# Optimization experiments

Hardware: AMD Instinct MI355X
Metric: run time of the kernel (lower is better)

## Reference

```python
import jax, jax.numpy as jnp
import numpy as np

SCALES = (1, 2, 4)
KS = 5          # conv kernel size
POOL = 2        # maxpool kernel & stride


def coarse_grain(x, s):
    # non-overlapping mean pool along last axis
    B, C, L = x.shape
    Lc = L // s
    return x[:, :, : Lc * s].reshape(B, C, Lc, s).mean(axis=-1)


def conv1d(x, w, b):
    # x: [B, C_in, L], w: [C_out, C_in, K] (torch layout), VALID padding, stride 1
    y = jax.lax.conv_general_dilated(
        x, w, window_strides=(1,), padding='VALID',
        dimension_numbers=('NCH', 'OIH', 'NCH'))
    return y + b[None, :, None]


def maxpool1d(x, k):
    B, C, L = x.shape
    Lp = L // k
    return x[:, :, : Lp * k].reshape(B, C, Lp, k).max(axis=-1)


def conv_block(x, w1, b1, w2, b2):
    x = maxpool1d(jax.nn.relu(conv1d(x, w1, b1)), POOL)
    x = maxpool1d(jax.nn.relu(conv1d(x, w2, b2)), POOL)
    return x


def setup_inputs() -> dict:
    key = jax.random.key(0)
    ks = jax.random.split(key, 9)
    B, C, NWL = 2048, 4, 480
    C1, C2 = 16, 32
    # flatten size per model's own arithmetic: sum over scales of conv/pool output lens * C2
    F = (117 + 57 + 27) * C2  # 6432
    NOUT = 5
    sc = lambda fan_in: 1.0 / np.sqrt(fan_in)
    return {
        'x':  jax.random.normal(ks[0], (B, C, NWL), dtype=jnp.float32),
        'w1': jax.random.uniform(ks[1], (C1, C, KS), jnp.float32, -sc(C * KS), sc(C * KS)),
        'b1': jax.random.uniform(ks[2], (C1,), jnp.float32, -sc(C * KS), sc(C * KS)),
        'w2': jax.random.uniform(ks[3], (C2, C1, KS), jnp.float32, -sc(C1 * KS), sc(C1 * KS)),
        'b2': jax.random.uniform(ks[4], (C2,), jnp.float32, -sc(C1 * KS), sc(C1 * KS)),
        'wl': jax.random.uniform(ks[5], (F, F), jnp.float32, -sc(F), sc(F)),
        'bl': jax.random.uniform(ks[6], (F,), jnp.float32, -sc(F), sc(F)),
        'wo': jax.random.uniform(ks[7], (NOUT, F), jnp.float32, -sc(F), sc(F)),
        'bo': jax.random.uniform(ks[8], (NOUT,), jnp.float32, -sc(F), sc(F)),
    }


def reference(x, w1, b1, w2, b2, wl, bl, wo, bo):
    # multi-scale feature mapping: shared ConvBlock applied to each coarse-grained scale
    feats = [conv_block(coarse_grain(x, s), w1, b1, w2, b2) for s in SCALES]
    f = jnp.concatenate(feats, axis=-1)            # [B, 32, 201]
    f = f.reshape(f.shape[0], -1)                  # [B, 6432]
    # the SAME linear layer (shared weights) is applied 4 times in torch
    for _ in range(4):
        f = jax.nn.relu(f @ wl.T + bl)
    return f @ wo.T + bo                           # [B, 5]
```

## Files before the change

### kernel.cpp

```cpp
#include <hip/hip_runtime.h>

typedef _Float16 v8h __attribute__((ext_vector_type(8)));
typedef _Float16 v4h __attribute__((ext_vector_type(4)));
typedef float    v4f __attribute__((ext_vector_type(4)));

#define GK 6432
#define GN 6432
#define GM 2048
#define KP 6528

__global__ void convert_w(const float* __restrict__ wl, _Float16* __restrict__ Wh)
{
    const int row = blockIdx.y;
    const int col = (blockIdx.x * 256 + threadIdx.x) * 4;
    if (col >= KP) return;
    v4h h;
    if (col < GK) {
        const float4 f = *(const float4*)(wl + (long)row * GK + col);
        h[0] = (_Float16)f.x; h[1] = (_Float16)f.y;
        h[2] = (_Float16)f.z; h[3] = (_Float16)f.w;
    } else {
        h[0] = (_Float16)0.f; h[1] = (_Float16)0.f;
        h[2] = (_Float16)0.f; h[3] = (_Float16)0.f;
    }
    *(v4h*)(Wh + (long)row * KP + col) = h;
}

#define SX   0
#define SX2  2048
#define SX4  3136
#define SW1  3712
#define SB1  4032
#define SW2  4048
#define SB2  6608
#define SP1  6640
#define LDSZ 13808

__global__ __launch_bounds__(256) void conv_feat(
    const float* __restrict__ x,
    const float* __restrict__ w1, const float* __restrict__ b1,
    const float* __restrict__ w2, const float* __restrict__ b2,
    _Float16* __restrict__ F0)
{
    __shared__ float lds[LDSZ];
    const int tid = threadIdx.x;
    const long b  = blockIdx.x;

    for (int i = tid; i < 1920; i += 256) {
        int c = i / 480, t = i % 480;
        lds[SX + c * 512 + t] = x[(b * 4 + c) * 480 + t];
    }
    for (int i = tid; i < 320;  i += 256) lds[SW1 + i] = w1[i];
    for (int i = tid; i < 16;   i += 256) lds[SB1 + i] = b1[i];
    for (int i = tid; i < 2560; i += 256) lds[SW2 + i] = w2[i];
    for (int i = tid; i < 32;   i += 256) lds[SB2 + i] = b2[i];
    for (int i = tid; i < KP - GK; i += 256) F0[b * KP + GK + i] = (_Float16)0.f;
    __syncthreads();

    for (int i = tid; i < 960; i += 256) {
        int c = i / 240, t = i % 240;
        lds[SX2 + c * 272 + t] = 0.5f * (lds[SX + c * 512 + 2 * t] + lds[SX + c * 512 + 2 * t + 1]);
    }
    for (int i = tid; i < 480; i += 256) {
        int c = i / 120, t = i % 120;
        float s = lds[SX + c * 512 + 4 * t]     + lds[SX + c * 512 + 4 * t + 1]
                + lds[SX + c * 512 + 4 * t + 2] + lds[SX + c * 512 + 4 * t + 3];
        lds[SX4 + c * 144 + t] = 0.25f * s;
    }
    __syncthreads();

    for (int jid = tid; jid < 16 * 34; jid += 256) {
        const int c1 = jid / 34, rid = jid % 34;
        const int sidx = (rid < 19) ? 0 : (rid < 29 ? 1 : 2);
        const int r0   = (sidx == 0) ? rid : (sidx == 1 ? rid - 19 : rid - 29);
        const int u0   = r0 * 13;
        const int xbase  = (sidx == 0) ? SX  : (sidx == 1 ? SX2 : SX4);
        const int xpitch = (sidx == 0) ? 512 : (sidx == 1 ? 272 : 144);
        const int P      = (sidx == 0) ? 238 : (sidx == 1 ? 118 : 58);
        const int pofs   = (sidx == 0) ? 0   : (sidx == 1 ? 238 : 356);

        float acc[26];
        const float bias = lds[SB1 + c1];
        #pragma unroll
        for (int i = 0; i < 26; ++i) acc[i] = bias;

        #pragma unroll
        for (int ci = 0; ci < 4; ++ci) {
            float w[30];
            const float* xr = &lds[xbase + ci * xpitch + 2 * u0];
            #pragma unroll
            for (int q = 0; q < 15; ++q) {
                float2 t2 = *(const float2*)(xr + 2 * q);
                w[2 * q] = t2.x; w[2 * q + 1] = t2.y;
            }
            float wt[5];
            #pragma unroll
            for (int k = 0; k < 5; ++k) wt[k] = lds[SW1 + (c1 * 4 + ci) * 5 + k];
            #pragma unroll
            for (int i = 0; i < 26; ++i) {
                #pragma unroll
                for (int k = 0; k < 5; ++k) acc[i] += w[i + k] * wt[k];
            }
        }
        #pragma unroll
        for (int i = 0; i < 13; ++i) {
            int u = u0 + i;
            if (u < P)
                lds[SP1 + c1 * 448 + pofs + u] = fmaxf(fmaxf(acc[2 * i], acc[2 * i + 1]), 0.f);
        }
    }
    __syncthreads();

    for (int jid = tid; jid < 32 * 17; jid += 256) {
        const int c2 = jid / 17, rid = jid % 17;
        const int sidx = (rid < 9) ? 0 : (rid < 14 ? 1 : 2);
        const int r0   = (sidx == 0) ? rid : (sidx == 1 ? rid - 9 : rid - 14);
        const int v0   = r0 * 13;
        const int pbase = (sidx == 0) ? 0   : (sidx == 1 ? 238 : 356);
        const int Pv    = (sidx == 0) ? 117 : (sidx == 1 ? 57  : 27);
        const int vout  = (sidx == 0) ? 0   : (sidx == 1 ? 117 : 174);

        float acc[26];
        const float bias = lds[SB2 + c2];
        #pragma unroll
        for (int i = 0; i < 26; ++i) acc[i] = bias;

        for (int c1 = 0; c1 < 16; ++c1) {
            float w[30];
            const float* pr = &lds[SP1 + c1 * 448 + pbase + 2 * v0];
            #pragma unroll
            for (int q = 0; q < 15; ++q) {
                float2 t2 = *(const float2*)(pr + 2 * q);
                w[2 * q] = t2.x; w[2 * q + 1] = t2.y;
            }
            float wt[5];
            #pragma unroll
            for (int k = 0; k < 5; ++k) wt[k] = lds[SW2 + (c2 * 16 + c1) * 5 + k];
            #pragma unroll
            for (int i = 0; i < 26; ++i) {
                #pragma unroll
                for (int k = 0; k < 5; ++k) acc[i] += w[i + k] * wt[k];
            }
        }
        #pragma unroll
        for (int i = 0; i < 13; ++i) {
            int v = v0 + i;
            if (v < Pv) {
                float f = fmaxf(fmaxf(acc[2 * i], acc[2 * i + 1]), 0.f);
                F0[b * KP + c2 * 201 + vout + v] = (_Float16)f;
            }
        }
    }
}

__global__ __launch_bounds__(1024, 4) void gemm16(
    const _Float16* __restrict__ A, const _Float16* __restrict__ Bw,
    const float* __restrict__ bias, _Float16* __restrict__ C)
{
    __shared__ _Float16 sA[2][256 * 64];
    __shared__ _Float16 sB[2][256 * 64];

    const int tid  = threadIdx.x;
    const int lane = tid & 63;
    const int wave = tid >> 6;
    const int wm   = wave >> 2;
    const int wn   = wave & 3;

    const int id = blockIdx.x;
    const long tile_m = (long)(id & 7) << 8;
    const long tile_n = (long)(id >> 3) << 8;

    const int lrow = lane >> 3;
    const int lcol = ((lane & 7) ^ lrow) << 3;

    const _Float16* pAst = A + (tile_m + wave * 16 + lrow) * (long)KP + lcol;
    const int dA0 = wave * 16 * 64, dA1 = dA0 + 512;

    const int bRow01 = (wave >> 2) * 64 + (wave & 3) * 8;
    long rb01 = tile_n + bRow01;
    long rb23 = rb01 + 32;
    long r01l = rb01 + lrow; if (r01l > 6431) r01l = 6431;
    long r23l = rb23 + lrow; if (r23l > 6431) r23l = 6431;
    const _Float16* pB01 = Bw + r01l * (long)KP + lcol;
    const _Float16* pB23 = Bw + r23l * (long)KP + lcol;
    const int dB01 = bRow01 * 64;
    const int dB23 = dB01 + 32 * 64;

#define GLD(p, d) __builtin_amdgcn_global_load_lds(                          \
        (const __attribute__((address_space(1))) void*)(p),                  \
        (__attribute__((address_space(3))) void*)(d), 16, 0, 0)

#define STAGE_A(CUR, q)   { GLD(q, &sA[CUR][dA0]); GLD((q) + 8L * KP, &sA[CUR][dA1]); }
#define STAGE_B01(CUR, q) { GLD(q, &sB[CUR][dB01]); }
#define STAGE_B23(CUR, q) { GLD(q, &sB[CUR][dB23]); }

    const int fr = lane & 15;
    const int fp = lane >> 4;
    const int sw = fr & 7;
    const int slot0 = ((fp)     ^ sw) << 3;
    const int slot1 = ((fp + 4) ^ sw) << 3;
    const int arow0 = wm * 64 + fr;
    const int brow0 = wn * 64 + fr;

    v8h af[4][2], bf0, bf1;
    v4f acc[4][4];
    #pragma unroll
    for (int mi = 0; mi < 4; ++mi) {
        #pragma unroll
        for (int nf = 0; nf < 4; ++nf) { v4f z = {0.f, 0.f, 0.f, 0.f}; acc[mi][nf] = z; }
    }

#define LDAALL(CUR) { _Pragma("unroll")                                      \
    for (int mi = 0; mi < 4; ++mi) {                                         \
        af[mi][0] = *(const v8h*)&sA[CUR][(arow0 + mi * 16) * 64 + slot0];   \
        af[mi][1] = *(const v8h*)&sA[CUR][(arow0 + mi * 16) * 64 + slot1];   \
    } }

#define LDB(CUR, P) {                                                        \
    bf0 = *(const v8h*)&sB[CUR][(brow0 + (P) * 16) * 64 + slot0];            \
    bf1 = *(const v8h*)&sB[CUR][(brow0 + (P) * 16) * 64 + slot1]; }

#define MMAP(P) { _Pragma("unroll")                                          \
    for (int mi = 0; mi < 4; ++mi) {                                         \
        acc[mi][P] = __builtin_amdgcn_mfma_f32_16x16x32_f16(af[mi][0], bf0,  \
                                                            acc[mi][P], 0, 0, 0); \
        acc[mi][P] = __builtin_amdgcn_mfma_f32_16x16x32_f16(af[mi][1], bf1,  \
                                                            acc[mi][P], 0, 0, 0); \
    } }

#define ROUND(CUR, S1, S2, VN) {                                             \
              \
    LDAALL(CUR); LDB(CUR, 0);                                                \
    if (S1) STAGE_B23((CUR) ^ 1, qB23);                                      \
    __builtin_amdgcn_s_barrier();                                            \
    asm volatile("s_waitcnt lgkmcnt(0)" ::: "memory");                       \
    __builtin_amdgcn_s_setprio(1);                                           \
    MMAP(0);                                                                 \
    __builtin_amdgcn_s_setprio(0);                                           \
    __builtin_amdgcn_s_barrier();                                            \
                             \
    LDB(CUR, 1);                                                             \
    if (S2) STAGE_A(CUR, qA);                                                \
    __builtin_amdgcn_s_barrier();                                            \
    asm volatile("s_waitcnt lgkmcnt(0)" ::: "memory");                       \
    __builtin_amdgcn_s_setprio(1);                                           \
    MMAP(1);                                                                 \
    __builtin_amdgcn_s_setprio(0);                                           \
    __builtin_amdgcn_s_barrier();                                            \
                          \
    LDB(CUR, 2);                                                             \
    if (S2) STAGE_B01(CUR, qB01);                                            \
    __builtin_amdgcn_s_barrier();                                            \
    asm volatile("s_waitcnt lgkmcnt(0)" ::: "memory");                       \
    __builtin_amdgcn_s_setprio(1);                                           \
    MMAP(2);                                                                 \
    __builtin_amdgcn_s_setprio(0);                                           \
    __builtin_amdgcn_s_barrier();                                            \
                                    \
    LDB(CUR, 3);                                                             \
    __builtin_amdgcn_s_barrier();                                            \
    asm volatile("s_waitcnt lgkmcnt(0)" ::: "memory");                       \
    __builtin_amdgcn_s_setprio(1);                                           \
    MMAP(3);                                                                 \
    __builtin_amdgcn_s_setprio(0);                                           \
    asm volatile("s_waitcnt vmcnt(" #VN ")" ::: "memory");                   \
    __builtin_amdgcn_s_barrier();                                            \
    qA += 64; qB01 += 64; qB23 += 64; }

    STAGE_A(0, pAst); STAGE_B01(0, pB01); STAGE_B23(0, pB23);
    STAGE_A(1, pAst + 64); STAGE_B01(1, pB01 + 64);
    asm volatile("s_waitcnt vmcnt(3)" ::: "memory");
    __builtin_amdgcn_s_barrier();

    const _Float16* qA   = pAst + 128;
    const _Float16* qB01 = pB01 + 128;
    const _Float16* qB23 = pB23 + 64;

    for (int kt = 0; kt < 100; kt += 2) {
        ROUND(0, 1, 1, 3);
        ROUND(1, 1, 1, 3);
    }
    ROUND(0, 1, 0, 0);
    ROUND(1, 0, 0, 0);

    #pragma unroll
    for (int nf = 0; nf < 4; ++nf) {
        const long col = tile_n + wn * 64 + nf * 16 + fr;
        if (col < KP) {
            const bool val = col < GN;
            const float bv = val ? bias[col] : 0.f;
            #pragma unroll
            for (int mi = 0; mi < 4; ++mi) {
                const long row = tile_m + wm * 64 + mi * 16 + fp * 4;
                #pragma unroll
                for (int r = 0; r < 4; ++r) {
                    float v = acc[mi][nf][r] + bv;
                    v = v > 0.f ? v : 0.f;
                    C[(row + r) * (long)KP + col] = val ? (_Float16)v : (_Float16)0.f;
                }
            }
        }
    }

#undef GLD
#undef STAGE_A
#undef STAGE_B01
#undef STAGE_B23
#undef LDAALL
#undef LDB
#undef MMAP
#undef ROUND
}

__global__ __launch_bounds__(256) void final_out(
    const _Float16* __restrict__ F, const float* __restrict__ wo,
    const float* __restrict__ bo, float* __restrict__ out)
{
    __shared__ float red[4][8];
    const long b   = blockIdx.x;
    const int tid  = threadIdx.x;
    const int lane = tid & 63;
    const int wave = tid >> 6;
    float acc[5] = {0.f, 0.f, 0.f, 0.f, 0.f};
    const _Float16* f = F + b * KP;

    const int c1 = (wave + 1) * 402;
    for (int c = wave * 402 + lane; c < c1; c += 64) {
        const int k = c << 2;
        v4h f4 = *(const v4h*)(f + k);
        const float f0 = (float)f4[0], f1 = (float)f4[1];
        const float f2 = (float)f4[2], f3 = (float)f4[3];
        #pragma unroll
        for (int o = 0; o < 5; ++o) {
            const float4 w4 = *(const float4*)(wo + o * GK + k);
            acc[o] += f0 * w4.x + f1 * w4.y + f2 * w4.z + f3 * w4.w;
        }
    }
    #pragma unroll
    for (int o = 0; o < 5; ++o) {
        #pragma unroll
        for (int off = 32; off > 0; off >>= 1) acc[o] += __shfl_down(acc[o], off, 64);
    }
    if (lane == 0) {
        #pragma unroll
        for (int o = 0; o < 5; ++o) red[wave][o] = acc[o];
    }
    __syncthreads();
    if (tid < 5)
        out[b * 5 + tid] = red[0][tid] + red[1][tid] + red[2][tid] + red[3][tid] + bo[tid];
}

extern "C" void kernel_launch(void* const* d_in, const int* in_sizes, int n_in,
                              void* d_out, int out_size, void* d_ws, size_t ws_size,
                              hipStream_t stream)
{
    const float* x  = (const float*)d_in[0];
    const float* w1 = (const float*)d_in[1];
    const float* b1 = (const float*)d_in[2];
    const float* w2 = (const float*)d_in[3];
    const float* b2 = (const float*)d_in[4];
    const float* wl = (const float*)d_in[5];
    const float* bl = (const float*)d_in[6];
    const float* wo = (const float*)d_in[7];
    const float* bo = (const float*)d_in[8];
    float* out = (float*)d_out;

    char* ws = (char*)d_ws;
    _Float16* Wh = (_Float16*)ws;
    _Float16* F0 = (_Float16*)(ws + 83976192);
    _Float16* F1 = (_Float16*)(ws + 83976192 + 26738688);

    convert_w<<<dim3(7, GN), 256, 0, stream>>>(wl, Wh);
    conv_feat<<<GM, 256, 0, stream>>>(x, w1, b1, w2, b2, F0);
    gemm16<<<208, 1024, 0, stream>>>(F0, Wh, bl, F1);
    gemm16<<<208, 1024, 0, stream>>>(F1, Wh, bl, F0);
    gemm16<<<208, 1024, 0, stream>>>(F0, Wh, bl, F1);
    gemm16<<<208, 1024, 0, stream>>>(F1, Wh, bl, F0);
    final_out<<<GM, 256, 0, stream>>>(F0, wo, bo, out);
}
```

Before: 1.179 ms.

## Fuse output projection into last GEMM epilogue and double-buffer B fragments

The final linear layer (5 outputs) moves into the epilogue of the fourth GEMM. Each tile applies bias and ReLU, dots the result with the wo slice staged in LDS, reduces across lanes, and atomically adds into an output that a small init kernel first fills with the bias. This removes the last activation write and the separate final_out kernel. The GEMM main loop also now loads the next B fragment into a second register pair before the current MFMAs and waits with lgkmcnt(2) instead of 0, overlapping LDS reads with matrix math. The cost is extra registers, nondeterministic float atomic summation order, and an added launch.

Measured after the change: 1.950 ms. +65.4%, slower.

```diff
diff --git a/kernel.cpp b/kernel.cpp
--- a/kernel.cpp
+++ b/kernel.cpp
@@ -153,9 +153,18 @@
     }
 }
 
+__global__ __launch_bounds__(512) void out_init(const float* __restrict__ bo,
+                                                float* __restrict__ out)
+{
+    const int i = blockIdx.x * 512 + threadIdx.x;
+    if (i < GM * 5) out[i] = bo[i % 5];
+}
+
+template<int FUSED>
 __global__ __launch_bounds__(1024, 4) void gemm16(
     const _Float16* __restrict__ A, const _Float16* __restrict__ Bw,
-    const float* __restrict__ bias, _Float16* __restrict__ C)
+    const float* __restrict__ bias, _Float16* __restrict__ C,
+    const float* __restrict__ wo, float* __restrict__ outp)
 {
     __shared__ _Float16 sA[2][256 * 64];
     __shared__ _Float16 sB[2][256 * 64];
@@ -202,7 +211,7 @@
     const int arow0 = wm * 64 + fr;
     const int brow0 = wn * 64 + fr;
 
-    v8h af[4][2], bf0, bf1;
+    v8h af[4][2], bA0, bA1, bB0, bB1;
     v4f acc[4][4];
     #pragma unroll
     for (int mi = 0; mi < 4; ++mi) {
@@ -216,52 +225,50 @@
         af[mi][1] = *(const v8h*)&sA[CUR][(arow0 + mi * 16) * 64 + slot1];   \
     } }
 
-#define LDB(CUR, P) {                                                        \
-    bf0 = *(const v8h*)&sB[CUR][(brow0 + (P) * 16) * 64 + slot0];            \
-    bf1 = *(const v8h*)&sB[CUR][(brow0 + (P) * 16) * 64 + slot1]; }
-
-#define MMAP(P) { _Pragma("unroll")                                          \
+#define LDB(CUR, P, D0, D1) {                                                \
+    D0 = *(const v8h*)&sB[CUR][(brow0 + (P) * 16) * 64 + slot0];             \
+    D1 = *(const v8h*)&sB[CUR][(brow0 + (P) * 16) * 64 + slot1]; }
+
+#define MMAP(P, B0, B1) { _Pragma("unroll")                                  \
     for (int mi = 0; mi < 4; ++mi) {                                         \
-        acc[mi][P] = __builtin_amdgcn_mfma_f32_16x16x32_f16(af[mi][0], bf0,  \
+        acc[mi][P] = __builtin_amdgcn_mfma_f32_16x16x32_f16(af[mi][0], B0,   \
                                                             acc[mi][P], 0, 0, 0); \
-        acc[mi][P] = __builtin_amdgcn_mfma_f32_16x16x32_f16(af[mi][1], bf1,  \
+        acc[mi][P] = __builtin_amdgcn_mfma_f32_16x16x32_f16(af[mi][1], B1,   \
                                                             acc[mi][P], 0, 0, 0); \
     } }
 
 #define ROUND(CUR, S1, S2, VN) {                                             \
-              \
-    LDAALL(CUR); LDB(CUR, 0);                                                \
+            \
+    LDAALL(CUR); LDB(CUR, 0, bA0, bA1); LDB(CUR, 1, bB0, bB1);               \
     if (S1) STAGE_B23((CUR) ^ 1, qB23);                                      \
     __builtin_amdgcn_s_barrier();                                            \
+    asm volatile("s_waitcnt lgkmcnt(2)" ::: "memory");                       \
+    __builtin_amdgcn_s_setprio(1);                                           \
+    MMAP(0, bA0, bA1);                                                       \
+    __builtin_amdgcn_s_setprio(0);                                           \
+    __builtin_amdgcn_s_barrier();                                            \
+                   \
+    LDB(CUR, 2, bA0, bA1);                                                   \
+    if (S2) STAGE_A(CUR, qA);                                                \
+    __builtin_amdgcn_s_barrier();                                            \
+    asm volatile("s_waitcnt lgkmcnt(2)" ::: "memory");                       \
+    __builtin_amdgcn_s_setprio(1);                                           \
+    MMAP(1, bB0, bB1);                                                       \
+    __builtin_amdgcn_s_setprio(0);                                           \
+    __builtin_amdgcn_s_barrier();                                            \
+                 \
+    LDB(CUR, 3, bB0, bB1);                                                   \
+    if (S2) STAGE_B01(CUR, qB01);                                            \
+    __builtin_amdgcn_s_barrier();                                            \
+    asm volatile("s_waitcnt lgkmcnt(2)" ::: "memory");                       \
+    __builtin_amdgcn_s_setprio(1);                                           \
+    MMAP(2, bA0, bA1);                                                       \
+    __builtin_amdgcn_s_setprio(0);                                           \
+    __builtin_amdgcn_s_barrier();                                            \
+               \
     asm volatile("s_waitcnt lgkmcnt(0)" ::: "memory");                       \
     __builtin_amdgcn_s_setprio(1);                                           \
-    MMAP(0);                                                                 \
-    __builtin_amdgcn_s_setprio(0);                                           \
-    __builtin_amdgcn_s_barrier();                                            \
-                             \
-    LDB(CUR, 1);                                                             \
-    if (S2) STAGE_A(CUR, qA);                                                \
-    __builtin_amdgcn_s_barrier();                                            \
-    asm volatile("s_waitcnt lgkmcnt(0)" ::: "memory");                       \
-    __builtin_amdgcn_s_setprio(1);                                           \
-    MMAP(1);                                                                 \
-    __builtin_amdgcn_s_setprio(0);                                           \
-    __builtin_amdgcn_s_barrier();                                            \
-                          \
-    LDB(CUR, 2);                                                             \
-    if (S2) STAGE_B01(CUR, qB01);                                            \
-    __builtin_amdgcn_s_barrier();                                            \
-    asm volatile("s_waitcnt lgkmcnt(0)" ::: "memory");                       \
-    __builtin_amdgcn_s_setprio(1);                                           \
-    MMAP(2);                                                                 \
-    __builtin_amdgcn_s_setprio(0);                                           \
-    __builtin_amdgcn_s_barrier();                                            \
-                                    \
-    LDB(CUR, 3);                                                             \
-    __builtin_amdgcn_s_barrier();                                            \
-    asm volatile("s_waitcnt lgkmcnt(0)" ::: "memory");                       \
-    __builtin_amdgcn_s_setprio(1);                                           \
-    MMAP(3);                                                                 \
+    MMAP(3, bB0, bB1);                                                       \
     __builtin_amdgcn_s_setprio(0);                                           \
     asm volatile("s_waitcnt vmcnt(" #VN ")" ::: "memory");                   \
     __builtin_amdgcn_s_barrier();                                            \
@@ -283,20 +290,69 @@
     ROUND(0, 1, 0, 0);
     ROUND(1, 0, 0, 0);
 
-    #pragma unroll
-    for (int nf = 0; nf < 4; ++nf) {
-        const long col = tile_n + wn * 64 + nf * 16 + fr;
-        if (col < KP) {
-            const bool val = col < GN;
-            const float bv = val ? bias[col] : 0.f;
-            #pragma unroll
-            for (int mi = 0; mi < 4; ++mi) {
-                const long row = tile_m + wm * 64 + mi * 16 + fp * 4;
-                #pragma unroll
-                for (int r = 0; r < 4; ++r) {
-                    float v = acc[mi][nf][r] + bv;
+    if constexpr (FUSED == 0) {
+        #pragma unroll
+        for (int nf = 0; nf < 4; ++nf) {
+            const long col = tile_n + wn * 64 + nf * 16 + fr;
+            if (col < KP) {
+                const bool val = col < GN;
+                const float bv = val ? bias[col] : 0.f;
+                #pragma unroll
+                for (int mi = 0; mi < 4; ++mi) {
+                    const long row = tile_m + wm * 64 + mi * 16 + fp * 4;
+                    #pragma unroll
+                    for (int r = 0; r < 4; ++r) {
+                        float v = acc[mi][nf][r] + bv;
+                        v = v > 0.f ? v : 0.f;
+                        C[(row + r) * (long)KP + col] = val ? (_Float16)v : (_Float16)0.f;
+                    }
+                }
+            }
+        }
+    } else {
+        float* fl = (float*)&sA[0][0];
+        __syncthreads();
+        for (int i = tid; i < 256 * 6; i += 1024) {
+            const int c = i & 255, j = i >> 8;
+            const long gcol = tile_n + c;
+            float v = 0.f;
+            if (gcol < GN) v = (j == 0) ? bias[gcol] : wo[(long)(j - 1) * GK + gcol];
+            fl[j * 256 + c] = v;
+        }
+        __syncthreads();
+        const float* biasL = fl;
+        const float* woL   = fl + 256;
+        #pragma unroll
+        for (int mi = 0; mi < 4; ++mi) {
+            #pragma unroll
+            for (int r = 0; r < 4; ++r) {
+                float s0 = 0.f, s1 = 0.f, s2 = 0.f, s3 = 0.f, s4 = 0.f;
+                #pragma unroll
+                for (int nf = 0; nf < 4; ++nf) {
+                    const int cl = wn * 64 + nf * 16 + fr;
+                    float v = acc[mi][nf][r] + biasL[cl];
                     v = v > 0.f ? v : 0.f;
-                    C[(row + r) * (long)KP + col] = val ? (_Float16)v : (_Float16)0.f;
+                    s0 += v * woL[cl];
+                    s1 += v * woL[256 + cl];
+                    s2 += v * woL[512 + cl];
+                    s3 += v * woL[768 + cl];
+                    s4 += v * woL[1024 + cl];
+                }
+                #pragma unroll
+                for (int m = 1; m < 16; m <<= 1) {
+                    s0 += __shfl_xor(s0, m, 64);
+                    s1 += __shfl_xor(s1, m, 64);
+                    s2 += __shfl_xor(s2, m, 64);
+                    s3 += __shfl_xor(s3, m, 64);
+                    s4 += __shfl_xor(s4, m, 64);
+                }
+                if (fr == 0) {
+                    const long row = tile_m + wm * 64 + mi * 16 + fp * 4 + r;
+                    atomicAdd(&outp[row * 5 + 0], s0);
+                    atomicAdd(&outp[row * 5 + 1], s1);
+                    atomicAdd(&outp[row * 5 + 2], s2);
+                    atomicAdd(&outp[row * 5 + 3], s3);
+                    atomicAdd(&outp[row * 5 + 4], s4);
                 }
             }
         }
@@ -310,44 +366,6 @@
 #undef LDB
 #undef MMAP
 #undef ROUND
-}
-
-__global__ __launch_bounds__(256) void final_out(
-    const _Float16* __restrict__ F, const float* __restrict__ wo,
-    const float* __restrict__ bo, float* __restrict__ out)
-{
-    __shared__ float red[4][8];
-    const long b   = blockIdx.x;
-    const int tid  = threadIdx.x;
-    const int lane = tid & 63;
-    const int wave = tid >> 6;
-    float acc[5] = {0.f, 0.f, 0.f, 0.f, 0.f};
-    const _Float16* f = F + b * KP;
-
-    const int c1 = (wave + 1) * 402;
-    for (int c = wave * 402 + lane; c < c1; c += 64) {
-        const int k = c << 2;
-        v4h f4 = *(const v4h*)(f + k);
-        const float f0 = (float)f4[0], f1 = (float)f4[1];
-        const float f2 = (float)f4[2], f3 = (float)f4[3];
-        #pragma unroll
-        for (int o = 0; o < 5; ++o) {
-            const float4 w4 = *(const float4*)(wo + o * GK + k);
-            acc[o] += f0 * w4.x + f1 * w4.y + f2 * w4.z + f3 * w4.w;
-        }
-    }
-    #pragma unroll
-    for (int o = 0; o < 5; ++o) {
-        #pragma unroll
-        for (int off = 32; off > 0; off >>= 1) acc[o] += __shfl_down(acc[o], off, 64);
-    }
-    if (lane == 0) {
-        #pragma unroll
-        for (int o = 0; o < 5; ++o) red[wave][o] = acc[o];
-    }
-    __syncthreads();
-    if (tid < 5)
-        out[b * 5 + tid] = red[0][tid] + red[1][tid] + red[2][tid] + red[3][tid] + bo[tid];
 }
 
 extern "C" void kernel_launch(void* const* d_in, const int* in_sizes, int n_in,
@@ -372,9 +390,9 @@
 
     convert_w<<<dim3(7, GN), 256, 0, stream>>>(wl, Wh);
     conv_feat<<<GM, 256, 0, stream>>>(x, w1, b1, w2, b2, F0);
-    gemm16<<<208, 1024, 0, stream>>>(F0, Wh, bl, F1);
-    gemm16<<<208, 1024, 0, stream>>>(F1, Wh, bl, F0);
-    gemm16<<<208, 1024, 0, stream>>>(F0, Wh, bl, F1);
-    gemm16<<<208, 1024, 0, stream>>>(F1, Wh, bl, F0);
-    final_out<<<GM, 256, 0, stream>>>(F0, wo, bo, out);
-}
+    gemm16<0><<<208, 1024, 0, stream>>>(F0, Wh, bl, F1, nullptr, nullptr);
+    gemm16<0><<<208, 1024, 0, stream>>>(F1, Wh, bl, F0, nullptr, nullptr);
+    gemm16<0><<<208, 1024, 0, stream>>>(F0, Wh, bl, F1, nullptr, nullptr);
+    out_init<<<20, 512, 0, stream>>>(bo, out);
+    gemm16<1><<<208, 1024, 0, stream>>>(F1, Wh, bl, nullptr, wo, out);
+}
```
